# Performance work log

Measured on AMD Instinct MI355X. Metric: run time of the kernel, lower is better.

Reference implementation:

```python
import jax, jax.numpy as jnp
import numpy as np


def setup_inputs() -> dict:
    key = jax.random.key(0)
    ks = jax.random.split(key, 4)
    B, T, D, H, E = 4, 2048, 1024, 4096, 8
    s = 0.02
    x = jax.random.normal(ks[0], (B, T, D), dtype=jnp.float32)
    Wr = jax.random.normal(ks[1], (D, E), dtype=jnp.float32) * s
    br = jnp.zeros((E,), dtype=jnp.float32)
    W1 = jax.random.normal(ks[2], (E, D, H), dtype=jnp.float32) * s
    b1 = jnp.zeros((E, H), dtype=jnp.float32)
    W2 = jax.random.normal(ks[3], (E, H, D), dtype=jnp.float32) * s
    b2 = jnp.zeros((E, D), dtype=jnp.float32)
    return {"x": x, "Wr": Wr, "br": br, "W1": W1, "b1": b1, "W2": W2, "b2": b2}


def reference(x, Wr, br, W1, b1, W2, b2):
    # Router: top-1 selection
    logits = jnp.einsum('btd,de->bte', x, Wr) + br            # [B,T,E]
    probs = jax.nn.softmax(logits, axis=-1)                   # [B,T,E]
    expert_idx = jnp.argmax(probs, axis=-1)                   # [B,T] int
    E = W1.shape[0]
    onehot = jax.nn.one_hot(expert_idx, E, dtype=x.dtype)     # [B,T,E]
    # Dense grouped-MLP over all experts, then combine with one-hot routing.
    # h: [B,E,T,H]
    h = jax.nn.relu(jnp.einsum('btd,edh->beth', x, W1) + b1[None, :, None, :])
    y = jnp.einsum('beth,ehd->betd', h, W2) + b2[None, :, None, :]  # [B,E,T,D]
    out = jnp.einsum('bte,betd->btd', onehot, y)              # [B,T,D]
    return out, probs, expert_idx
```

## Files before the change

kernel.cpp:

```cpp
#include <hip/hip_runtime.h>

#define NTOK 8192
#define DD 1024
#define HH 4096
#define EE 8
#define MAXBLK 72

typedef __attribute__((ext_vector_type(8))) short bf16x8;
typedef __attribute__((ext_vector_type(4))) float f32x4;

__device__ __forceinline__ unsigned short f2bf(float f) {
  unsigned u = __builtin_bit_cast(unsigned, f);
  u += 0x7fffu + ((u >> 16) & 1u);
  return (unsigned short)(u >> 16);
}

union Pack8 {
  unsigned short u[8];
  uint4 v;
};

__device__ __forceinline__ void gload_lds16(const void* g, void* l) {
  __builtin_amdgcn_global_load_lds(
      (const __attribute__((address_space(1))) unsigned int*)g,
      (__attribute__((address_space(3))) unsigned int*)l, 16, 0, 0);
}

__global__ __launch_bounds__(256) void k_router(
    const float* __restrict__ x, const float* __restrict__ Wr,
    const float* __restrict__ br, float* __restrict__ probs,
    float* __restrict__ idxf, int* __restrict__ idxi,
    unsigned short* __restrict__ xb) {
  const int lane = threadIdx.x & 63;
  const int token = blockIdx.x * 4 + (threadIdx.x >> 6);
  const float* xr = x + (size_t)token * DD;

  float acc[EE];
#pragma unroll
  for (int e = 0; e < EE; ++e) acc[e] = 0.f;

#pragma unroll
  for (int i = 0; i < 4; ++i) {
    const int d0 = i * 256 + lane * 4;
    const float4 xv = *reinterpret_cast<const float4*>(xr + d0);
    union { unsigned short u[4]; uint2 v; } pk;
    pk.u[0] = f2bf(xv.x); pk.u[1] = f2bf(xv.y);
    pk.u[2] = f2bf(xv.z); pk.u[3] = f2bf(xv.w);
    *reinterpret_cast<uint2*>(xb + (size_t)token * DD + d0) = pk.v;
    const float xs[4] = {xv.x, xv.y, xv.z, xv.w};
#pragma unroll
    for (int j = 0; j < 4; ++j) {
      const float xd = xs[j];
      const float4 w0 = *reinterpret_cast<const float4*>(Wr + (size_t)(d0 + j) * EE);
      const float4 w1 = *reinterpret_cast<const float4*>(Wr + (size_t)(d0 + j) * EE + 4);
      acc[0] += xd * w0.x; acc[1] += xd * w0.y; acc[2] += xd * w0.z; acc[3] += xd * w0.w;
      acc[4] += xd * w1.x; acc[5] += xd * w1.y; acc[6] += xd * w1.z; acc[7] += xd * w1.w;
    }
  }
#pragma unroll
  for (int s = 32; s > 0; s >>= 1) {
#pragma unroll
    for (int e = 0; e < EE; ++e) acc[e] += __shfl_xor(acc[e], s, 64);
  }

  float lg[EE];
#pragma unroll
  for (int e = 0; e < EE; ++e) lg[e] = acc[e] + br[e];

  int best = 0;
  float bv = lg[0];
#pragma unroll
  for (int e = 1; e < EE; ++e) {
    if (lg[e] > bv) { bv = lg[e]; best = e; }
  }
  float p[EE], s = 0.f;
#pragma unroll
  for (int e = 0; e < EE; ++e) { p[e] = expf(lg[e] - bv); s += p[e]; }
  const float inv = 1.f / s;

  if (lane == 0) {
#pragma unroll
    for (int e = 0; e < EE; ++e) probs[(size_t)token * EE + e] = p[e] * inv;
    idxf[token] = (float)best;
    idxi[token] = best;
  }
}

__global__ __launch_bounds__(512) void k_compact(const int* __restrict__ idxi,
                                                 int* __restrict__ cnt,
                                                 int* __restrict__ off,
                                                 int* __restrict__ sorted,
                                                 int* __restrict__ meta) {
  __shared__ int sidx[NTOK];
  __shared__ int scnt[EE], soff[EE];
  const int tid = threadIdx.x;
  for (int i = tid; i < NTOK; i += 512) sidx[i] = idxi[i];
  __syncthreads();
  const int w = tid >> 6, lane = tid & 63;
  if (w < EE) {
    int c = 0;
    for (int i = 0; i < NTOK / 64; ++i) {
      unsigned long long m = __ballot(sidx[i * 64 + lane] == w);
      c += __popcll(m);
    }
    if (lane == 0) scnt[w] = c;
  }
  __syncthreads();
  if (tid == 0) {
    int s = 0;
    for (int e = 0; e < EE; ++e) { soff[e] = s; s += scnt[e]; }
    int nb = 0;
    for (int e = 0; e < EE; ++e) {
      const int nmb = (scnt[e] + 127) >> 7;
      for (int m = 0; m < nmb; ++m) {
        meta[16 + nb] = e;
        meta[96 + nb] = m << 7;
        ++nb;
      }
    }
    meta[0] = nb;
  }
  __syncthreads();
  if (w < EE) {
    int base = soff[w];
    const unsigned long long ltmask = (1ull << lane) - 1ull;
    for (int i = 0; i < NTOK / 64; ++i) {
      const int tok = i * 64 + lane;
      const bool f = (sidx[tok] == w);
      unsigned long long m = __ballot(f);
      if (f) {
        int r = __popcll(m & ltmask);
        sorted[base + r] = tok;
      }
      base += __popcll(m);
    }
    if (lane == 0) { cnt[w] = scnt[w]; off[w] = soff[w]; }
  }
}

__global__ __launch_bounds__(256) void k_trcvt64(const float* __restrict__ in,
                                                 unsigned short* __restrict__ outp,
                                                 int R, int C) {
  const int e = blockIdx.z;
  const int r0 = blockIdx.y * 64, c0 = blockIdx.x * 64;
  const float* src = in + (size_t)e * R * C + (size_t)r0 * C + c0;
  unsigned short* dst = outp + (size_t)e * R * C + (size_t)c0 * R + r0;
  __shared__ unsigned short t[64 * 66];
  const int tid = threadIdx.x;
#pragma unroll
  for (int it = 0; it < 4; ++it) {
    const int r = it * 16 + (tid >> 4), c4 = (tid & 15) * 4;
    const float4 v = *reinterpret_cast<const float4*>(src + (size_t)r * C + c4);
    t[r * 66 + c4 + 0] = f2bf(v.x);
    t[r * 66 + c4 + 1] = f2bf(v.y);
    t[r * 66 + c4 + 2] = f2bf(v.z);
    t[r * 66 + c4 + 3] = f2bf(v.w);
  }
  __syncthreads();
#pragma unroll
  for (int it = 0; it < 2; ++it) {
    const int cc = it * 32 + (tid >> 3), r8 = (tid & 7) * 8;
    Pack8 p;
#pragma unroll
    for (int j = 0; j < 8; ++j) p.u[j] = t[(r8 + j) * 66 + cc];
    *reinterpret_cast<uint4*>(dst + (size_t)cc * R + r8) = p.v;
  }
}

__global__ __launch_bounds__(256) void k_gemm1n(
    const unsigned short* __restrict__ xb, const unsigned short* __restrict__ W1t,
    const float* __restrict__ b1, const int* __restrict__ meta,
    const int* __restrict__ cnt, const int* __restrict__ off,
    const int* __restrict__ sorted, unsigned short* __restrict__ h) {
  const int bid = blockIdx.y;
  if (bid >= meta[0]) return;
  const int e = meta[16 + bid];
  const int m0 = meta[96 + bid];
  const int c = cnt[e], base = off[e];
  const int n0 = blockIdx.x * 128;

  __shared__ __align__(16) unsigned short Al[128 * 64];
  __shared__ __align__(16) unsigned short Bl[128 * 64];

  const int tid = threadIdx.x, l = tid & 63, w = tid >> 6;

  const unsigned short* aptr[4];
  const unsigned short* bptr[4];
  int soff4[4];
#pragma unroll
  for (int i = 0; i < 4; ++i) {
    const int r = i * 32 + w * 8 + (l >> 3);
    const int swz = ((l & 7) ^ (r & 7)) * 8;
    int ar = m0 + r; if (ar >= c) ar = c - 1;
    const int tok = sorted[base + ar];
    aptr[i] = xb + (size_t)tok * DD + swz;
    bptr[i] = W1t + ((size_t)e * HH + n0 + r) * DD + swz;
    soff4[i] = r * 64 + (l & 7) * 8;
  }

  const int lr = l & 15, lg = l >> 4;
  const int wr = w >> 1, wc = w & 1;
  int aoff[4], boff[4], asw[4], bsw[4];
#pragma unroll
  for (int m = 0; m < 4; ++m) {
    int row = wr * 64 + m * 16 + lr;
    aoff[m] = row * 64; asw[m] = row & 7;
    row = wc * 64 + m * 16 + lr;
    boff[m] = row * 64; bsw[m] = row & 7;
  }

  f32x4 acc[4][4];
#pragma unroll
  for (int m = 0; m < 4; ++m)
#pragma unroll
    for (int n = 0; n < 4; ++n) acc[m][n] = {0.f, 0.f, 0.f, 0.f};

  for (int k0 = 0; k0 < DD; k0 += 64) {
    __syncthreads();
#pragma unroll
    for (int i = 0; i < 4; ++i) gload_lds16(aptr[i] + k0, &Al[soff4[i]]);
#pragma unroll
    for (int i = 0; i < 4; ++i) gload_lds16(bptr[i] + k0, &Bl[soff4[i]]);
    __syncthreads();
#pragma unroll
    for (int ks = 0; ks < 2; ++ks) {
      bf16x8 af[4], bv[4];
#pragma unroll
      for (int m = 0; m < 4; ++m)
        af[m] = *reinterpret_cast<const bf16x8*>(&Al[aoff[m] + (((ks * 4 + lg) ^ asw[m]) * 8)]);
#pragma unroll
      for (int n = 0; n < 4; ++n)
        bv[n] = *reinterpret_cast<const bf16x8*>(&Bl[boff[n] + (((ks * 4 + lg) ^ bsw[n]) * 8)]);
#pragma unroll
      for (int m = 0; m < 4; ++m)
#pragma unroll
        for (int n = 0; n < 4; ++n)
          acc[m][n] = __builtin_amdgcn_mfma_f32_16x16x32_bf16(af[m], bv[n], acc[m][n], 0, 0, 0);
    }
  }

  const int valid = c - m0;
#pragma unroll
  for (int m = 0; m < 4; ++m) {
#pragma unroll
    for (int rr = 0; rr < 4; ++rr) {
      const int tr = wr * 64 + m * 16 + lg * 4 + rr;
      if (tr < valid) {
        const size_t row = (size_t)(base + m0 + tr);
#pragma unroll
        for (int n = 0; n < 4; ++n) {
          const int col = n0 + wc * 64 + n * 16 + lr;
          const float v = acc[m][n][rr] + b1[e * HH + col];
          h[row * HH + col] = f2bf(fmaxf(v, 0.f));
        }
      }
    }
  }
}

__global__ __launch_bounds__(256) void k_gemm2w(
    const unsigned short* __restrict__ h, const unsigned short* __restrict__ W2t,
    const float* __restrict__ b2, const int* __restrict__ meta,
    const int* __restrict__ cnt, const int* __restrict__ off,
    const int* __restrict__ sorted, float* __restrict__ out) {
  const int bid = blockIdx.y;
  if (bid >= meta[0]) return;
  const int e = meta[16 + bid];
  const int m0 = meta[96 + bid];
  const int c = cnt[e], base = off[e];
  const int n0 = blockIdx.x * 64;

  __shared__ __align__(16) unsigned short Al[128 * 64];
  __shared__ __align__(16) unsigned short Bl[64 * 64];

  const int tid = threadIdx.x, l = tid & 63, w = tid >> 6;

  const unsigned short* aptr[4];
  const unsigned short* bptr[2];
  int asoff[4], bsoff[2];
#pragma unroll
  for (int i = 0; i < 4; ++i) {
    const int r = i * 32 + w * 8 + (l >> 3);
    const int swz = ((l & 7) ^ (r & 7)) * 8;
    int ar = m0 + r; if (ar >= c) ar = c - 1;
    aptr[i] = h + (size_t)(base + ar) * HH + swz;
    asoff[i] = r * 64 + (l & 7) * 8;
  }
#pragma unroll
  for (int i = 0; i < 2; ++i) {
    const int r = i * 32 + w * 8 + (l >> 3);
    const int swz = ((l & 7) ^ (r & 7)) * 8;
    bptr[i] = W2t + ((size_t)e * DD + n0 + r) * HH + swz;
    bsoff[i] = r * 64 + (l & 7) * 8;
  }

  const int lr = l & 15, lg = l >> 4;
  const int wr = w >> 1, wc = w & 1;
  int aoff[4], boff[2], asw[4], bsw[2];
#pragma unroll
  for (int m = 0; m < 4; ++m) {
    const int row = wr * 64 + m * 16 + lr;
    aoff[m] = row * 64; asw[m] = row & 7;
  }
#pragma unroll
  for (int n = 0; n < 2; ++n) {
    const int row = wc * 32 + n * 16 + lr;
    boff[n] = row * 64; bsw[n] = row & 7;
  }

  f32x4 acc[4][2];
#pragma unroll
  for (int m = 0; m < 4; ++m)
#pragma unroll
    for (int n = 0; n < 2; ++n) acc[m][n] = {0.f, 0.f, 0.f, 0.f};

  for (int k0 = 0; k0 < HH; k0 += 64) {
    __syncthreads();
#pragma unroll
    for (int i = 0; i < 4; ++i) gload_lds16(aptr[i] + k0, &Al[asoff[i]]);
#pragma unroll
    for (int i = 0; i < 2; ++i) gload_lds16(bptr[i] + k0, &Bl[bsoff[i]]);
    __syncthreads();
#pragma unroll
    for (int ks = 0; ks < 2; ++ks) {
      bf16x8 af[4], bv[2];
#pragma unroll
      for (int m = 0; m < 4; ++m)
        af[m] = *reinterpret_cast<const bf16x8*>(&Al[aoff[m] + (((ks * 4 + lg) ^ asw[m]) * 8)]);
#pragma unroll
      for (int n = 0; n < 2; ++n)
        bv[n] = *reinterpret_cast<const bf16x8*>(&Bl[boff[n] + (((ks * 4 + lg) ^ bsw[n]) * 8)]);
#pragma unroll
      for (int m = 0; m < 4; ++m)
#pragma unroll
        for (int n = 0; n < 2; ++n)
          acc[m][n] = __builtin_amdgcn_mfma_f32_16x16x32_bf16(af[m], bv[n], acc[m][n], 0, 0, 0);
    }
  }

  const int valid = c - m0;
#pragma unroll
  for (int m = 0; m < 4; ++m) {
#pragma unroll
    for (int rr = 0; rr < 4; ++rr) {
      const int tr = wr * 64 + m * 16 + lg * 4 + rr;
      if (tr < valid) {
        const int token = sorted[base + m0 + tr];
#pragma unroll
        for (int n = 0; n < 2; ++n) {
          const int col = n0 + wc * 32 + n * 16 + lr;
          out[(size_t)token * DD + col] = acc[m][n][rr] + b2[e * DD + col];
        }
      }
    }
  }
}

extern "C" void kernel_launch(void* const* d_in, const int* in_sizes, int n_in,
                              void* d_out, int out_size, void* d_ws, size_t ws_size,
                              hipStream_t stream) {
  const float* x  = (const float*)d_in[0];
  const float* Wr = (const float*)d_in[1];
  const float* br = (const float*)d_in[2];
  const float* W1 = (const float*)d_in[3];
  const float* b1 = (const float*)d_in[4];
  const float* W2 = (const float*)d_in[5];
  const float* b2 = (const float*)d_in[6];

  float* out   = (float*)d_out;
  float* probs = out + (size_t)NTOK * DD;
  float* idxf  = probs + (size_t)NTOK * EE;

  char* ws = (char*)d_ws;
  int* cnt    = (int*)(ws + 0);
  int* off    = (int*)(ws + 64);
  int* meta   = (int*)(ws + 128);
  int* idxi   = (int*)(ws + 1024);
  int* sorted = (int*)(ws + 33792);

  const size_t OFF_XB  = 66560;
  const size_t OFF_W1T = OFF_XB + (size_t)NTOK * DD * 2;
  const size_t OFF_H   = OFF_W1T + (size_t)EE * DD * HH * 2;
  const size_t OFF_W2T = OFF_XB;

  unsigned short* xb  = (unsigned short*)(ws + OFF_XB);
  unsigned short* W1t = (unsigned short*)(ws + OFF_W1T);
  unsigned short* W2t = (unsigned short*)(ws + OFF_W2T);
  unsigned short* h   = (unsigned short*)(ws + OFF_H);

  k_router<<<NTOK / 4, 256, 0, stream>>>(x, Wr, br, probs, idxf, idxi, xb);
  k_compact<<<1, 512, 0, stream>>>(idxi, cnt, off, sorted, meta);
  k_trcvt64<<<dim3(HH / 64, DD / 64, EE), 256, 0, stream>>>(W1, W1t, DD, HH);
  k_gemm1n<<<dim3(HH / 128, MAXBLK), 256, 0, stream>>>(xb, W1t, b1, meta, cnt, off, sorted, h);
  k_trcvt64<<<dim3(DD / 64, HH / 64, EE), 256, 0, stream>>>(W2, W2t, HH, DD);
  k_gemm2w<<<dim3(DD / 64, MAXBLK), 256, 0, stream>>>(h, W2t, b2, meta, cnt, off, sorted, out);
}
```

Baseline: 375.0 us.

## Triple-buffer LDS in second expert GEMM with async prefetch pipeline

```diff
diff --git a/kernel.cpp b/kernel.cpp
--- a/kernel.cpp
+++ b/kernel.cpp
@@ -5,6 +5,7 @@
 #define HH 4096
 #define EE 8
 #define MAXBLK 72
+#define NT2 64
 
 typedef __attribute__((ext_vector_type(8))) short bf16x8;
 typedef __attribute__((ext_vector_type(4))) float f32x4;
@@ -258,7 +259,7 @@
   }
 }
 
-__global__ __launch_bounds__(256) void k_gemm2w(
+__global__ __launch_bounds__(256) void k_gemm2p(
     const unsigned short* __restrict__ h, const unsigned short* __restrict__ W2t,
     const float* __restrict__ b2, const int* __restrict__ meta,
     const int* __restrict__ cnt, const int* __restrict__ off,
@@ -270,8 +271,8 @@
   const int c = cnt[e], base = off[e];
   const int n0 = blockIdx.x * 64;
 
-  __shared__ __align__(16) unsigned short Al[128 * 64];
-  __shared__ __align__(16) unsigned short Bl[64 * 64];
+  __shared__ __align__(16) unsigned short Al[3][128 * 64];
+  __shared__ __align__(16) unsigned short Bl[3][64 * 64];
 
   const int tid = threadIdx.x, l = tid & 63, w = tid >> 6;
 
@@ -314,29 +315,55 @@
 #pragma unroll
     for (int n = 0; n < 2; ++n) acc[m][n] = {0.f, 0.f, 0.f, 0.f};
 
-  for (int k0 = 0; k0 < HH; k0 += 64) {
-    __syncthreads();
-#pragma unroll
-    for (int i = 0; i < 4; ++i) gload_lds16(aptr[i] + k0, &Al[asoff[i]]);
-#pragma unroll
-    for (int i = 0; i < 2; ++i) gload_lds16(bptr[i] + k0, &Bl[bsoff[i]]);
-    __syncthreads();
-#pragma unroll
-    for (int ks = 0; ks < 2; ++ks) {
-      bf16x8 af[4], bv[2];
-#pragma unroll
-      for (int m = 0; m < 4; ++m)
-        af[m] = *reinterpret_cast<const bf16x8*>(&Al[aoff[m] + (((ks * 4 + lg) ^ asw[m]) * 8)]);
-#pragma unroll
-      for (int n = 0; n < 2; ++n)
-        bv[n] = *reinterpret_cast<const bf16x8*>(&Bl[boff[n] + (((ks * 4 + lg) ^ bsw[n]) * 8)]);
-#pragma unroll
-      for (int m = 0; m < 4; ++m)
-#pragma unroll
-        for (int n = 0; n < 2; ++n)
-          acc[m][n] = __builtin_amdgcn_mfma_f32_16x16x32_bf16(af[m], bv[n], acc[m][n], 0, 0, 0);
-    }
-  }
+#define STAGE2(buf, kk)                                                    \
+  {                                                                        \
+    _Pragma("unroll") for (int i = 0; i < 4; ++i)                          \
+        gload_lds16(aptr[i] + (kk), &Al[buf][asoff[i]]);                   \
+    _Pragma("unroll") for (int i = 0; i < 2; ++i)                          \
+        gload_lds16(bptr[i] + (kk), &Bl[buf][bsoff[i]]);                   \
+  }
+
+#define COMPUTE2(buf)                                                      \
+  {                                                                        \
+    _Pragma("unroll") for (int ks = 0; ks < 2; ++ks) {                     \
+      bf16x8 af[4], bv[2];                                                 \
+      _Pragma("unroll") for (int m = 0; m < 4; ++m)                        \
+          af[m] = *reinterpret_cast<const bf16x8*>(                        \
+              &Al[buf][aoff[m] + (((ks * 4 + lg) ^ asw[m]) * 8)]);         \
+      _Pragma("unroll") for (int n = 0; n < 2; ++n)                        \
+          bv[n] = *reinterpret_cast<const bf16x8*>(                        \
+              &Bl[buf][boff[n] + (((ks * 4 + lg) ^ bsw[n]) * 8)]);         \
+      _Pragma("unroll") for (int m = 0; m < 4; ++m)                        \
+          _Pragma("unroll") for (int n = 0; n < 2; ++n)                    \
+              acc[m][n] = __builtin_amdgcn_mfma_f32_16x16x32_bf16(         \
+                  af[m], bv[n], acc[m][n], 0, 0, 0);                       \
+    }                                                                      \
+  }
+
+  STAGE2(0, 0);
+  STAGE2(1, 64);
+
+  int bufc = 0;
+#pragma unroll 1
+  for (int t = 0; t < NT2 - 2; ++t) {
+    asm volatile("s_waitcnt vmcnt(6)" ::: "memory");
+    __builtin_amdgcn_s_barrier();
+    COMPUTE2(bufc);
+    __builtin_amdgcn_s_barrier();
+    int bn = bufc + 2; if (bn >= 3) bn -= 3;
+    STAGE2(bn, (t + 2) * 64);
+    bufc = (bufc + 1 == 3) ? 0 : bufc + 1;
+  }
+  asm volatile("s_waitcnt vmcnt(6)" ::: "memory");
+  __builtin_amdgcn_s_barrier();
+  COMPUTE2(bufc);
+  bufc = (bufc + 1 == 3) ? 0 : bufc + 1;
+  asm volatile("s_waitcnt vmcnt(0)" ::: "memory");
+  __builtin_amdgcn_s_barrier();
+  COMPUTE2(bufc);
+
+#undef STAGE2
+#undef COMPUTE2
 
   const int valid = c - m0;
 #pragma unroll
@@ -393,5 +420,5 @@
   k_trcvt64<<<dim3(HH / 64, DD / 64, EE), 256, 0, stream>>>(W1, W1t, DD, HH);
   k_gemm1n<<<dim3(HH / 128, MAXBLK), 256, 0, stream>>>(xb, W1t, b1, meta, cnt, off, sorted, h);
   k_trcvt64<<<dim3(DD / 64, HH / 64, EE), 256, 0, stream>>>(W2, W2t, HH, DD);
-  k_gemm2w<<<dim3(DD / 64, MAXBLK), 256, 0, stream>>>(h, W2t, b2, meta, cnt, off, sorted, out);
-}
+  k_gemm2p<<<dim3(DD / 64, MAXBLK), 256, 0, stream>>>(h, W2t, b2, meta, cnt, off, sorted, out);
+}
```

Result: slower. 399.9 us (+6.6%).

## Split-K the second expert GEMM in two halves with a reduction pass

Applied to the files above, without the earlier changes.

```diff
diff --git a/kernel.cpp b/kernel.cpp
--- a/kernel.cpp
+++ b/kernel.cpp
@@ -258,17 +258,21 @@
   }
 }
 
-__global__ __launch_bounds__(256) void k_gemm2w(
+template <int KH>
+__global__ __launch_bounds__(256) void k_gemm2s(
     const unsigned short* __restrict__ h, const unsigned short* __restrict__ W2t,
     const float* __restrict__ b2, const int* __restrict__ meta,
     const int* __restrict__ cnt, const int* __restrict__ off,
-    const int* __restrict__ sorted, float* __restrict__ out) {
+    const int* __restrict__ sorted, float* __restrict__ out,
+    float* __restrict__ scr) {
   const int bid = blockIdx.y;
   if (bid >= meta[0]) return;
   const int e = meta[16 + bid];
   const int m0 = meta[96 + bid];
   const int c = cnt[e], base = off[e];
   const int n0 = blockIdx.x * 64;
+  const int kh = (KH == 2) ? blockIdx.z : 0;
+  const int kbase = kh * (HH / KH);
 
   __shared__ __align__(16) unsigned short Al[128 * 64];
   __shared__ __align__(16) unsigned short Bl[64 * 64];
@@ -283,14 +287,14 @@
     const int r = i * 32 + w * 8 + (l >> 3);
     const int swz = ((l & 7) ^ (r & 7)) * 8;
     int ar = m0 + r; if (ar >= c) ar = c - 1;
-    aptr[i] = h + (size_t)(base + ar) * HH + swz;
+    aptr[i] = h + (size_t)(base + ar) * HH + kbase + swz;
     asoff[i] = r * 64 + (l & 7) * 8;
   }
 #pragma unroll
   for (int i = 0; i < 2; ++i) {
     const int r = i * 32 + w * 8 + (l >> 3);
     const int swz = ((l & 7) ^ (r & 7)) * 8;
-    bptr[i] = W2t + ((size_t)e * DD + n0 + r) * HH + swz;
+    bptr[i] = W2t + ((size_t)e * DD + n0 + r) * HH + kbase + swz;
     bsoff[i] = r * 64 + (l & 7) * 8;
   }
 
@@ -314,7 +318,7 @@
 #pragma unroll
     for (int n = 0; n < 2; ++n) acc[m][n] = {0.f, 0.f, 0.f, 0.f};
 
-  for (int k0 = 0; k0 < HH; k0 += 64) {
+  for (int k0 = 0; k0 < HH / KH; k0 += 64) {
     __syncthreads();
 #pragma unroll
     for (int i = 0; i < 4; ++i) gload_lds16(aptr[i] + k0, &Al[asoff[i]]);
@@ -338,6 +342,7 @@
     }
   }
 
+  float* dst = (KH == 2 && blockIdx.z == 1) ? scr : out;
   const int valid = c - m0;
 #pragma unroll
   for (int m = 0; m < 4; ++m) {
@@ -349,11 +354,32 @@
 #pragma unroll
         for (int n = 0; n < 2; ++n) {
           const int col = n0 + wc * 32 + n * 16 + lr;
-          out[(size_t)token * DD + col] = acc[m][n][rr] + b2[e * DD + col];
+          float v = acc[m][n][rr];
+          if (KH == 1) v += b2[e * DD + col];
+          dst[(size_t)token * DD + col] = v;
         }
       }
     }
   }
+}
+
+__global__ __launch_bounds__(256) void k_reduce2(float* __restrict__ out,
+                                                 const float* __restrict__ scr,
+                                                 const float* __restrict__ b2,
+                                                 const int* __restrict__ idxi) {
+  const size_t f = (size_t)blockIdx.x * 256 + threadIdx.x;
+  const int token = (int)(f >> 8);
+  const int d4 = ((int)f & 255) * 4;
+  const int e = idxi[token];
+  const float4 a = *reinterpret_cast<const float4*>(out + f * 4);
+  const float4 b = *reinterpret_cast<const float4*>(scr + f * 4);
+  const float4 bb = *reinterpret_cast<const float4*>(b2 + (size_t)e * DD + d4);
+  float4 r;
+  r.x = a.x + b.x + bb.x;
+  r.y = a.y + b.y + bb.y;
+  r.z = a.z + b.z + bb.z;
+  r.w = a.w + b.w + bb.w;
+  *reinterpret_cast<float4*>(out + f * 4) = r;
 }
 
 extern "C" void kernel_launch(void* const* d_in, const int* in_sizes, int n_in,
@@ -382,16 +408,27 @@
   const size_t OFF_W1T = OFF_XB + (size_t)NTOK * DD * 2;
   const size_t OFF_H   = OFF_W1T + (size_t)EE * DD * HH * 2;
   const size_t OFF_W2T = OFF_XB;
+  const size_t OFF_SCR = OFF_H + (size_t)NTOK * HH * 2;
+  const size_t NEED_SPLIT = OFF_SCR + (size_t)NTOK * DD * 4;
 
   unsigned short* xb  = (unsigned short*)(ws + OFF_XB);
   unsigned short* W1t = (unsigned short*)(ws + OFF_W1T);
   unsigned short* W2t = (unsigned short*)(ws + OFF_W2T);
   unsigned short* h   = (unsigned short*)(ws + OFF_H);
+  float*          scr = (float*)(ws + OFF_SCR);
 
   k_router<<<NTOK / 4, 256, 0, stream>>>(x, Wr, br, probs, idxf, idxi, xb);
   k_compact<<<1, 512, 0, stream>>>(idxi, cnt, off, sorted, meta);
   k_trcvt64<<<dim3(HH / 64, DD / 64, EE), 256, 0, stream>>>(W1, W1t, DD, HH);
   k_gemm1n<<<dim3(HH / 128, MAXBLK), 256, 0, stream>>>(xb, W1t, b1, meta, cnt, off, sorted, h);
   k_trcvt64<<<dim3(DD / 64, HH / 64, EE), 256, 0, stream>>>(W2, W2t, HH, DD);
-  k_gemm2w<<<dim3(DD / 64, MAXBLK), 256, 0, stream>>>(h, W2t, b2, meta, cnt, off, sorted, out);
-}
+
+  if (ws_size >= NEED_SPLIT) {
+    k_gemm2s<2><<<dim3(DD / 64, MAXBLK, 2), 256, 0, stream>>>(
+        h, W2t, b2, meta, cnt, off, sorted, out, scr);
+    k_reduce2<<<(NTOK * DD) / (256 * 4), 256, 0, stream>>>(out, scr, b2, idxi);
+  } else {
+    k_gemm2s<1><<<dim3(DD / 64, MAXBLK, 1), 256, 0, stream>>>(
+        h, W2t, b2, meta, cnt, off, sorted, out, scr);
+  }
+}
```

New measurement: 389.4 us. 1.04x slower.
